# Kernel tuning notes

Hardware: AMD Instinct MI355X
Metric: run time of the kernel (lower is better)

The kernel has to match this reference:

```python
import jax, jax.numpy as jnp
import numpy as np

B, LAT, FCON, NCOND = 1024, 64, 256, 1
HID, E, GATE_H = 512, 8, 64
FREC, NFUT = 256, 2
IN_SZ = LAT + FCON * NCOND          # 320
INTER = LAT + HID                   # 576
OUT_SZ = NFUT * FREC                # 512


def setup_inputs() -> dict:
    key = jax.random.key(0)
    ks = jax.random.split(key, 16)

    def kaiming(k, shape):
        # kaiming_uniform over fan_in = shape[-2] (matches torch init on [E, in, out])
        fan_in = shape[-2]
        bound = np.sqrt(6.0 / fan_in)
        return jax.random.uniform(k, shape, jnp.float32, -bound, bound)

    def lin(kw, kb, din, dout):
        bound = 1.0 / np.sqrt(din)
        w = jax.random.uniform(kw, (din, dout), jnp.float32, -bound, bound)
        b = jax.random.uniform(kb, (dout,), jnp.float32, -bound, bound)
        return w, b

    gw1, gb1 = lin(ks[0], ks[1], IN_SZ, GATE_H)
    gw2, gb2 = lin(ks[2], ks[3], GATE_H, GATE_H)
    gw3, gb3 = lin(ks[4], ks[5], GATE_H, E)

    return {
        "z": jax.random.normal(ks[6], (B, LAT), jnp.float32),
        "c": jax.random.normal(ks[7], (B, FCON * NCOND), jnp.float32),
        "w0": kaiming(ks[8], (E, IN_SZ, HID)),
        "b0": jnp.full((E, HID), 0.01, jnp.float32),
        "w1": kaiming(ks[9], (E, INTER, HID)),
        "b1": jnp.full((E, HID), 0.01, jnp.float32),
        "w2": kaiming(ks[10], (E, INTER, OUT_SZ)),
        "b2": jnp.full((E, OUT_SZ), 0.01, jnp.float32),
        "gw1": gw1, "gb1": gb1,
        "gw2": gw2, "gb2": gb2,
        "gw3": gw3, "gb3": gb3,
    }


def _moe_layer(coeff, z, layer_out, w, b, act):
    # math identical to: mixed_w = coeff @ flat(w); baddbmm(mixed_b, inp, mixed_w)
    # expressed as a fused contraction (no [B, in, out] materialization)
    inp = jnp.concatenate((z, layer_out), axis=1)          # [B, in]
    out = jnp.einsum('bi,eio,be->bo', inp, w, coeff)       # [B, out]
    out = out + coeff @ b                                  # mixed bias
    return act(out) if act is not None else out


def reference(z, c, w0, b0, w1, b1, w2, b2, gw1, gb1, gw2, gb2, gw3, gb3):
    x = jnp.concatenate((z, c), axis=1)                    # [B, IN_SZ]
    h = jax.nn.elu(x @ gw1 + gb1)
    h = jax.nn.elu(h @ gw2 + gb2)
    coeff = jax.nn.softmax(h @ gw3 + gb3, axis=1)          # [B, E]

    out = _moe_layer(coeff, z, c, w0, b0, jax.nn.elu)      # [B, HID]
    out = _moe_layer(coeff, z, out, w1, b1, jax.nn.elu)    # [B, HID]
    out = _moe_layer(coeff, z, out, w2, b2, None)          # [B, OUT_SZ]
    return out
```

## Files before the change

### kernel.cpp

```cpp
#include <hip/hip_runtime.h>
#include <hip/hip_bf16.h>
#include <stdint.h>
#include <math.h>

#define B_    1024
#define LAT   64
#define FCON  256
#define IN_SZ 320
#define HID   512
#define E_    8
#define GH    64
#define INTER 576
#define OUT_SZ 512
#define NTOT  4096
#define KI0   10
#define KI12  18

typedef __attribute__((ext_vector_type(8))) __bf16 bf16x8;
typedef __attribute__((ext_vector_type(4))) float  f32x4;

__device__ __forceinline__ float elu_f(float x) { return x > 0.f ? x : expf(x) - 1.f; }
__device__ __forceinline__ __bf16 to_bf16(float f) {
    __hip_bfloat16 h = __float2bfloat16(f);
    return *reinterpret_cast<__bf16*>(&h);
}


#define PREP_GATE 64
#define PREP_ZC   (PREP_GATE + 160)
#define PREP_W0   (PREP_ZC + 8 * KI0 * 2)
#define PREP_W1   (PREP_W0 + 8 * KI12 * 2)
#define PREP_W2   (PREP_W1 + 8 * KI12 * 2)
#define PREP_ALL  PREP_W2

#define WPAD 261
#define SMEM_F (32 * WPAD)

__device__ __forceinline__ void do_zcpack(
    int bx, const float* __restrict__ z, const float* __restrict__ c,
    bf16x8* __restrict__ Ap0, bf16x8* __restrict__ Ap1, bf16x8* __restrict__ Ap2)
{
    const int wid  = bx * 4 + (threadIdx.x >> 6);
    const int lane = threadIdx.x & 63, q = lane >> 4, r = lane & 15;
    bf16x8 v;
    if (wid < 128) {
        const int mi = wid >> 1, ki = wid & 1;
        const float* src = z + (size_t)(mi * 16 + r) * LAT + ki * 32 + q * 8;
        const f32x4 lo = *(const f32x4*)src, hi = *(const f32x4*)(src + 4);
#pragma unroll
        for (int j = 0; j < 4; j++) { v[j] = to_bf16(lo[j]); v[j + 4] = to_bf16(hi[j]); }
        Ap0[((size_t)mi * KI0  + ki) * 64 + lane] = v;
        Ap1[((size_t)mi * KI12 + ki) * 64 + lane] = v;
        Ap2[((size_t)mi * KI12 + ki) * 64 + lane] = v;
    } else {
        const int cid = wid - 128;
        const int mi = cid >> 3, ki = 2 + (cid & 7);
        const float* src = c + (size_t)(mi * 16 + r) * FCON + (ki - 2) * 32 + q * 8;
        const f32x4 lo = *(const f32x4*)src, hi = *(const f32x4*)(src + 4);
#pragma unroll
        for (int j = 0; j < 4; j++) { v[j] = to_bf16(lo[j]); v[j + 4] = to_bf16(hi[j]); }
        Ap0[((size_t)mi * KI0 + ki) * 64 + lane] = v;
    }
}

__device__ __forceinline__ void do_wpack2(
    int f, const float* __restrict__ w, bf16x8* __restrict__ Wp, int KI,
    float* __restrict__ lds)
{
    const int e = f / (2 * KI), rem = f % (2 * KI);
    const int ki = rem >> 1, ot2 = rem & 1;
    const int K = KI * 32;
    const float* base = w + ((size_t)e * K + ki * 32) * 512 + ot2 * 256;

#pragma unroll
    for (int p = 0; p < 8; ++p) {
        const int idx = p * 256 + threadIdx.x;
        const int kl = idx >> 6, c4 = idx & 63;
        const f32x4 v = *(const f32x4*)(base + (size_t)kl * 512 + c4 * 4);
        float* d = lds + kl * WPAD + c4 * 4;
        d[0] = v[0]; d[1] = v[1]; d[2] = v[2]; d[3] = v[3];
    }
    __syncthreads();

    const int wv = threadIdx.x >> 6, lane = threadIdx.x & 63;
    const int q = lane >> 4, r = lane & 15;
#pragma unroll
    for (int ff = 0; ff < 4; ++ff) {
        const int fo = wv * 4 + ff;
        const int ol = fo * 16 + r;
        bf16x8 v;
#pragma unroll
        for (int j = 0; j < 8; ++j) v[j] = to_bf16(lds[(q * 8 + j) * WPAD + ol]);
        const int ni = e * 32 + ot2 * 16 + fo;
        Wp[((size_t)ni * KI + ki) * 64 + lane] = v;
    }
}

__device__ __forceinline__ void do_gate(
    int bx, const float* __restrict__ z, const float* __restrict__ c,
    const float* __restrict__ gw1, const float* __restrict__ gb1,
    const float* __restrict__ gw2, const float* __restrict__ gb2,
    const float* __restrict__ gw3, const float* __restrict__ gb3,
    float* __restrict__ coeff, float* __restrict__ smem)
{
    float* xs = smem;
    float* h  = smem + 16 * 320;
    const int r0 = bx * 16;
    const int wave = threadIdx.x >> 6, lane = threadIdx.x & 63;

#pragma unroll
    for (int p = 0; p < 5; ++p) {
        const int idx = p * 256 + threadIdx.x;
        const int row = idx / 80, c4 = idx % 80;
        const float* src = (c4 < 16)
            ? (z + (size_t)(r0 + row) * LAT  + c4 * 4)
            : (c + (size_t)(r0 + row) * FCON + (c4 - 16) * 4);
        *(f32x4*)(xs + row * 320 + c4 * 4) = *(const f32x4*)src;
    }
    __syncthreads();

    float a0, a1, a2, a3;
    {
        const float b = gb1[lane];
        a0 = b; a1 = b; a2 = b; a3 = b;
        const float* x0 = xs + (wave * 4 + 0) * 320;
        const float* x1 = xs + (wave * 4 + 1) * 320;
        const float* x2 = xs + (wave * 4 + 2) * 320;
        const float* x3 = xs + (wave * 4 + 3) * 320;
#pragma unroll 8
        for (int i = 0; i < IN_SZ; ++i) {
            const float wv = gw1[i * GH + lane];
            a0 = fmaf(x0[i], wv, a0);
            a1 = fmaf(x1[i], wv, a1);
            a2 = fmaf(x2[i], wv, a2);
            a3 = fmaf(x3[i], wv, a3);
        }
        h[(wave * 4 + 0) * GH + lane] = elu_f(a0);
        h[(wave * 4 + 1) * GH + lane] = elu_f(a1);
        h[(wave * 4 + 2) * GH + lane] = elu_f(a2);
        h[(wave * 4 + 3) * GH + lane] = elu_f(a3);
    }
    {
        const float b = gb2[lane];
        a0 = b; a1 = b; a2 = b; a3 = b;
        const float* h0 = h + (wave * 4 + 0) * GH;
        const float* h1 = h + (wave * 4 + 1) * GH;
        const float* h2 = h + (wave * 4 + 2) * GH;
        const float* h3 = h + (wave * 4 + 3) * GH;
#pragma unroll 8
        for (int i = 0; i < GH; ++i) {
            const float wv = gw2[i * GH + lane];
            a0 = fmaf(h0[i], wv, a0);
            a1 = fmaf(h1[i], wv, a1);
            a2 = fmaf(h2[i], wv, a2);
            a3 = fmaf(h3[i], wv, a3);
        }
        h[(wave * 4 + 0) * GH + lane] = elu_f(a0);
        h[(wave * 4 + 1) * GH + lane] = elu_f(a1);
        h[(wave * 4 + 2) * GH + lane] = elu_f(a2);
        h[(wave * 4 + 3) * GH + lane] = elu_f(a3);
    }
    if (lane < 32) {
        const int rloc = lane >> 3, e = lane & 7;
        const float* hr = h + (wave * 4 + rloc) * GH;
        float lg = gb3[e];
#pragma unroll 8
        for (int i = 0; i < GH; ++i) lg = fmaf(hr[i], gw3[i * E_ + e], lg);
        float mx = lg;
        mx = fmaxf(mx, __shfl_xor(mx, 1, 8));
        mx = fmaxf(mx, __shfl_xor(mx, 2, 8));
        mx = fmaxf(mx, __shfl_xor(mx, 4, 8));
        const float ex = expf(lg - mx);
        float sm = ex;
        sm += __shfl_xor(sm, 1, 8);
        sm += __shfl_xor(sm, 2, 8);
        sm += __shfl_xor(sm, 4, 8);
        coeff[(size_t)(r0 + wave * 4 + rloc) * E_ + e] = ex / sm;
    }
}

__global__ __launch_bounds__(256) void prep_kernel(
    const float* __restrict__ z, const float* __restrict__ c,
    const float* __restrict__ w0, const float* __restrict__ w1,
    const float* __restrict__ w2,
    const float* __restrict__ gw1, const float* __restrict__ gb1,
    const float* __restrict__ gw2, const float* __restrict__ gb2,
    const float* __restrict__ gw3, const float* __restrict__ gb3,
    bf16x8* __restrict__ Ap0, bf16x8* __restrict__ Ap1, bf16x8* __restrict__ Ap2,
    bf16x8* __restrict__ Wp0, bf16x8* __restrict__ Wp1, bf16x8* __restrict__ Wp2,
    float* __restrict__ coeff)
{
    __shared__ float smem[SMEM_F];
    const int bx = blockIdx.x;
    if (bx < PREP_GATE) {
        do_gate(bx, z, c, gw1, gb1, gw2, gb2, gw3, gb3, coeff, smem);
    } else if (bx < PREP_ZC) {
        do_zcpack(bx - PREP_GATE, z, c, Ap0, Ap1, Ap2);
    } else if (bx < PREP_W0) {
        do_wpack2(bx - PREP_ZC, w0, Wp0, KI0, smem);
    } else if (bx < PREP_W1) {
        do_wpack2(bx - PREP_W0, w1, Wp1, KI12, smem);
    } else {
        do_wpack2(bx - PREP_W1, w2, Wp2, KI12, smem);
    }
}

template<int KI, int FINAL>
__global__ __launch_bounds__(512) void layer_kernel(
    const bf16x8* __restrict__ Ap, const bf16x8* __restrict__ Wp,
    const float* __restrict__ coeff, const float* __restrict__ bias,
    __bf16* __restrict__ ApN, float* __restrict__ fout)
{
    constexpr int KIH = KI / 2;
    __shared__ float sbuf[4][8][64];
    const int lane = threadIdx.x & 63, w = threadIdx.x >> 6;
    const int kh = w & 1, pp = w >> 1;
    const int q = lane >> 4, r = lane & 15;
    const int o0 = blockIdx.x * 16;
    const int nt = blockIdx.x;
    const int mi0 = blockIdx.y * 8 + pp * 2;

    const bf16x8* aB0 = Ap + ((size_t)(mi0 + 0) * KI + kh * KIH) * 64 + lane;
    const bf16x8* aB1 = Ap + ((size_t)(mi0 + 1) * KI + kh * KIH) * 64 + lane;
    const bf16x8* bB  = Wp + ((size_t)nt * KI + kh * KIH) * 64 + lane;

    f32x4 acc[2][E_];
#pragma unroll
    for (int u = 0; u < 2; u++)
#pragma unroll
        for (int e = 0; e < E_; e++) acc[u][e] = (f32x4){0.f, 0.f, 0.f, 0.f};

#pragma unroll
    for (int ki = 0; ki < KIH; ++ki) {
        const bf16x8 af0 = aB0[(size_t)ki * 64];
        const bf16x8 af1 = aB1[(size_t)ki * 64];
        bf16x8 bf[E_];
#pragma unroll
        for (int e = 0; e < E_; e++)
            bf[e] = bB[((size_t)e * 32 * KI + ki) * 64];
#pragma unroll
        for (int e = 0; e < E_; e++) {
            acc[0][e] = __builtin_amdgcn_mfma_f32_16x16x32_bf16(af0, bf[e], acc[0][e], 0, 0, 0);
            acc[1][e] = __builtin_amdgcn_mfma_f32_16x16x32_bf16(af1, bf[e], acc[1][e], 0, 0, 0);
        }
    }

    float be[E_];
#pragma unroll
    for (int e = 0; e < E_; e++)
        be[e] = kh ? 0.f : bias[(size_t)e * 512 + o0 + r];

    float s[2][4];
#pragma unroll
    for (int u = 0; u < 2; u++) {
#pragma unroll
        for (int v = 0; v < 4; v++) {
            const int row = (mi0 + u) * 16 + q * 4 + v;
            const float* cr = coeff + (size_t)row * E_;
            const f32x4 clo = *(const f32x4*)cr, chi = *(const f32x4*)(cr + 4);
            float sv = 0.f;
#pragma unroll
            for (int e = 0; e < 4; e++) sv += clo[e] * (acc[u][e][v] + be[e]);
#pragma unroll
            for (int e = 0; e < 4; e++) sv += chi[e] * (acc[u][4 + e][v] + be[4 + e]);
            s[u][v] = sv;
        }
    }

    if (kh) {
#pragma unroll
        for (int u = 0; u < 2; u++)
#pragma unroll
            for (int v = 0; v < 4; v++) sbuf[pp][u * 4 + v][lane] = s[u][v];
    }
    __syncthreads();
    if (!kh) {
#pragma unroll
        for (int u = 0; u < 2; u++) {
            const int mi = mi0 + u;
#pragma unroll
            for (int v = 0; v < 4; v++) {
                const int row = mi * 16 + q * 4 + v;
                const float t = s[u][v] + sbuf[pp][u * 4 + v][lane];
                if (FINAL) {
                    fout[(size_t)row * OUT_SZ + o0 + r] = t;
                } else {
                    const float hh = elu_f(t);
                    const int k  = LAT + o0 + r;
                    const int ki2 = k >> 5, kq2 = (k & 31) >> 3, jb2 = k & 7;
                    ApN[(((size_t)mi * KI12 + ki2) * 64 + kq2 * 16 + (q * 4 + v)) * 8 + jb2] =
                        to_bf16(hh);
                }
            }
        }
    }
}

static inline size_t align256(size_t x) { return (x + 255) & ~(size_t)255; }

extern "C" void kernel_launch(void* const* d_in, const int* in_sizes, int n_in,
                              void* d_out, int out_size, void* d_ws, size_t ws_size,
                              hipStream_t stream)
{
    const float* z   = (const float*)d_in[0];
    const float* c   = (const float*)d_in[1];
    const float* w0  = (const float*)d_in[2];
    const float* b0  = (const float*)d_in[3];
    const float* w1  = (const float*)d_in[4];
    const float* b1  = (const float*)d_in[5];
    const float* w2  = (const float*)d_in[6];
    const float* b2  = (const float*)d_in[7];
    const float* gw1 = (const float*)d_in[8];
    const float* gb1 = (const float*)d_in[9];
    const float* gw2 = (const float*)d_in[10];
    const float* gb2 = (const float*)d_in[11];
    const float* gw3 = (const float*)d_in[12];
    const float* gb3 = (const float*)d_in[13];
    float* out = (float*)d_out;

    uint8_t* p = (uint8_t*)d_ws;
    bf16x8* Wp0 = (bf16x8*)p; p += align256((size_t)NTOT * IN_SZ * 2);
    bf16x8* Wp1 = (bf16x8*)p; p += align256((size_t)NTOT * INTER * 2);
    bf16x8* Wp2 = (bf16x8*)p; p += align256((size_t)NTOT * INTER * 2);
    bf16x8* Ap0 = (bf16x8*)p; p += align256((size_t)B_ * IN_SZ * 2);
    bf16x8* Ap1 = (bf16x8*)p; p += align256((size_t)B_ * INTER * 2);
    bf16x8* Ap2 = (bf16x8*)p; p += align256((size_t)B_ * INTER * 2);
    float* coeff = (float*)p; p += align256((size_t)B_ * E_ * 4);

    prep_kernel<<<PREP_ALL, 256, 0, stream>>>(
        z, c, w0, w1, w2, gw1, gb1, gw2, gb2, gw3, gb3,
        Ap0, Ap1, Ap2, Wp0, Wp1, Wp2, coeff);

    layer_kernel<KI0, 0><<<dim3(32, 8), 512, 0, stream>>>(
        Ap0, Wp0, coeff, b0, (__bf16*)Ap1, nullptr);
    layer_kernel<KI12, 0><<<dim3(32, 8), 512, 0, stream>>>(
        Ap1, Wp1, coeff, b1, (__bf16*)Ap2, nullptr);
    layer_kernel<KI12, 1><<<dim3(32, 8), 512, 0, stream>>>(
        Ap2, Wp2, coeff, b2, nullptr, out);
}
```

Measured before the change: 161.0 us.

## Stage expert weights through LDS with async double-buffered loads in layer kernel

```diff
diff --git a/kernel.cpp b/kernel.cpp
--- a/kernel.cpp
+++ b/kernel.cpp
@@ -23,6 +23,13 @@
 __device__ __forceinline__ __bf16 to_bf16(float f) {
     __hip_bfloat16 h = __float2bfloat16(f);
     return *reinterpret_cast<__bf16*>(&h);
+}
+
+__device__ __forceinline__ void async_ld16(const void* g, void* l) {
+    __builtin_amdgcn_global_load_lds(
+        (const __attribute__((address_space(1))) unsigned int*)g,
+        (__attribute__((address_space(3))) unsigned int*)l,
+        16, 0, 0);
 }
 
 
@@ -206,92 +213,90 @@
 }
 
 template<int KI, int FINAL>
-__global__ __launch_bounds__(512) void layer_kernel(
+__global__ __launch_bounds__(256) void layer_kernel(
     const bf16x8* __restrict__ Ap, const bf16x8* __restrict__ Wp,
     const float* __restrict__ coeff, const float* __restrict__ bias,
     __bf16* __restrict__ ApN, float* __restrict__ fout)
 {
-    constexpr int KIH = KI / 2;
-    __shared__ float sbuf[4][8][64];
+    constexpr int NS = KI / 2;
+    __shared__ bf16x8 bs[2][2][E_][64];
     const int lane = threadIdx.x & 63, w = threadIdx.x >> 6;
-    const int kh = w & 1, pp = w >> 1;
     const int q = lane >> 4, r = lane & 15;
     const int o0 = blockIdx.x * 16;
     const int nt = blockIdx.x;
-    const int mi0 = blockIdx.y * 8 + pp * 2;
-
-    const bf16x8* aB0 = Ap + ((size_t)(mi0 + 0) * KI + kh * KIH) * 64 + lane;
-    const bf16x8* aB1 = Ap + ((size_t)(mi0 + 1) * KI + kh * KIH) * 64 + lane;
-    const bf16x8* bB  = Wp + ((size_t)nt * KI + kh * KIH) * 64 + lane;
-
-    f32x4 acc[2][E_];
-#pragma unroll
-    for (int u = 0; u < 2; u++)
-#pragma unroll
-        for (int e = 0; e < E_; e++) acc[u][e] = (f32x4){0.f, 0.f, 0.f, 0.f};
-
-#pragma unroll
-    for (int ki = 0; ki < KIH; ++ki) {
-        const bf16x8 af0 = aB0[(size_t)ki * 64];
-        const bf16x8 af1 = aB1[(size_t)ki * 64];
-        bf16x8 bf[E_];
-#pragma unroll
-        for (int e = 0; e < E_; e++)
-            bf[e] = bB[((size_t)e * 32 * KI + ki) * 64];
-#pragma unroll
-        for (int e = 0; e < E_; e++) {
-            acc[0][e] = __builtin_amdgcn_mfma_f32_16x16x32_bf16(af0, bf[e], acc[0][e], 0, 0, 0);
-            acc[1][e] = __builtin_amdgcn_mfma_f32_16x16x32_bf16(af1, bf[e], acc[1][e], 0, 0, 0);
-        }
-    }
+    const int mi = blockIdx.y * 4 + w;
+
+    const bf16x8* aB = Ap + (size_t)mi * KI * 64 + lane;
+    const int e0 = w * 2;
+
+    f32x4 acc[E_];
+#pragma unroll
+    for (int e = 0; e < E_; e++) acc[e] = (f32x4){0.f, 0.f, 0.f, 0.f};
+
+#define STAGE(s_, buf_)                                                        \
+    {                                                                          \
+        _Pragma("unroll")                                                      \
+        for (int kk = 0; kk < 2; ++kk) {                                       \
+            _Pragma("unroll")                                                  \
+            for (int t = 0; t < 2; ++t) {                                      \
+                const int e = e0 + t;                                          \
+                const bf16x8* g = Wp +                                         \
+                    ((size_t)e * 32 * KI + (size_t)nt * KI + ((s_) * 2 + kk)) * 64 + lane; \
+                async_ld16((const void*)g, (void*)&bs[buf_][kk][e][0]);        \
+            }                                                                  \
+        }                                                                      \
+    }
+
+    STAGE(0, 0);
+    bf16x8 af0 = aB[0], af1 = aB[64];
+    __syncthreads();
+
+    int cur = 0;
+#pragma unroll
+    for (int s = 0; s < NS; ++s) {
+        bf16x8 afn0 = af0, afn1 = af1;
+        if (s + 1 < NS) {
+            STAGE(s + 1, cur ^ 1);
+            afn0 = aB[(size_t)(s * 2 + 2) * 64];
+            afn1 = aB[(size_t)(s * 2 + 3) * 64];
+        }
+#pragma unroll
+        for (int kk = 0; kk < 2; ++kk) {
+            const bf16x8 af = kk ? af1 : af0;
+            bf16x8 bfr[E_];
+#pragma unroll
+            for (int e = 0; e < E_; e++) bfr[e] = bs[cur][kk][e][lane];
+#pragma unroll
+            for (int e = 0; e < E_; e++)
+                acc[e] = __builtin_amdgcn_mfma_f32_16x16x32_bf16(af, bfr[e], acc[e], 0, 0, 0);
+        }
+        __syncthreads();
+        af0 = afn0; af1 = afn1; cur ^= 1;
+    }
+#undef STAGE
 
     float be[E_];
 #pragma unroll
-    for (int e = 0; e < E_; e++)
-        be[e] = kh ? 0.f : bias[(size_t)e * 512 + o0 + r];
-
-    float s[2][4];
-#pragma unroll
-    for (int u = 0; u < 2; u++) {
-#pragma unroll
-        for (int v = 0; v < 4; v++) {
-            const int row = (mi0 + u) * 16 + q * 4 + v;
-            const float* cr = coeff + (size_t)row * E_;
-            const f32x4 clo = *(const f32x4*)cr, chi = *(const f32x4*)(cr + 4);
-            float sv = 0.f;
-#pragma unroll
-            for (int e = 0; e < 4; e++) sv += clo[e] * (acc[u][e][v] + be[e]);
-#pragma unroll
-            for (int e = 0; e < 4; e++) sv += chi[e] * (acc[u][4 + e][v] + be[4 + e]);
-            s[u][v] = sv;
-        }
-    }
-
-    if (kh) {
-#pragma unroll
-        for (int u = 0; u < 2; u++)
-#pragma unroll
-            for (int v = 0; v < 4; v++) sbuf[pp][u * 4 + v][lane] = s[u][v];
-    }
-    __syncthreads();
-    if (!kh) {
-#pragma unroll
-        for (int u = 0; u < 2; u++) {
-            const int mi = mi0 + u;
-#pragma unroll
-            for (int v = 0; v < 4; v++) {
-                const int row = mi * 16 + q * 4 + v;
-                const float t = s[u][v] + sbuf[pp][u * 4 + v][lane];
-                if (FINAL) {
-                    fout[(size_t)row * OUT_SZ + o0 + r] = t;
-                } else {
-                    const float hh = elu_f(t);
-                    const int k  = LAT + o0 + r;
-                    const int ki2 = k >> 5, kq2 = (k & 31) >> 3, jb2 = k & 7;
-                    ApN[(((size_t)mi * KI12 + ki2) * 64 + kq2 * 16 + (q * 4 + v)) * 8 + jb2] =
-                        to_bf16(hh);
-                }
-            }
+    for (int e = 0; e < E_; e++) be[e] = bias[(size_t)e * 512 + o0 + r];
+
+#pragma unroll
+    for (int v = 0; v < 4; v++) {
+        const int row = mi * 16 + q * 4 + v;
+        const float* cr = coeff + (size_t)row * E_;
+        const f32x4 clo = *(const f32x4*)cr, chi = *(const f32x4*)(cr + 4);
+        float sv = 0.f;
+#pragma unroll
+        for (int e = 0; e < 4; e++) sv += clo[e] * (acc[e][v] + be[e]);
+#pragma unroll
+        for (int e = 0; e < 4; e++) sv += chi[e] * (acc[4 + e][v] + be[4 + e]);
+        if (FINAL) {
+            fout[(size_t)row * OUT_SZ + o0 + r] = sv;
+        } else {
+            const float hh = elu_f(sv);
+            const int k  = LAT + o0 + r;
+            const int ki2 = k >> 5, kq2 = (k & 31) >> 3, jb2 = k & 7;
+            ApN[(((size_t)mi * KI12 + ki2) * 64 + kq2 * 16 + (q * 4 + v)) * 8 + jb2] =
+                to_bf16(hh);
         }
     }
 }
@@ -331,10 +336,10 @@
         z, c, w0, w1, w2, gw1, gb1, gw2, gb2, gw3, gb3,
         Ap0, Ap1, Ap2, Wp0, Wp1, Wp2, coeff);
 
-    layer_kernel<KI0, 0><<<dim3(32, 8), 512, 0, stream>>>(
+    layer_kernel<KI0, 0><<<dim3(32, 16), 256, 0, stream>>>(
         Ap0, Wp0, coeff, b0, (__bf16*)Ap1, nullptr);
-    layer_kernel<KI12, 0><<<dim3(32, 8), 512, 0, stream>>>(
+    layer_kernel<KI12, 0><<<dim3(32, 16), 256, 0, stream>>>(
         Ap1, Wp1, coeff, b1, (__bf16*)Ap2, nullptr);
-    layer_kernel<KI12, 1><<<dim3(32, 8), 512, 0, stream>>>(
+    layer_kernel<KI12, 1><<<dim3(32, 16), 256, 0, stream>>>(
         Ap2, Wp2, coeff, b2, nullptr, out);
 }
```

Result: faster. 137.7 us (-14.5%).
